# Kernel tuning notes

Hardware: AMD Instinct MI355X
Metric: run time of the kernel (lower is better)

Reference implementation:

```python
import jax, jax.numpy as jnp
import numpy as np

# Fixed feature-map grid sizes for a 640x480 input with strides (8,16,32)
LEVELS = [(8.0, 60, 80), (16.0, 30, 40), (32.0, 15, 20)]  # (stride, h, w) -> 6300 anchors
TOPK = 5


def make_anchors():
    pts, strs = [], []
    for stride, h, w in LEVELS:
        sx = np.arange(w, dtype=np.float32) + 0.5
        sy = np.arange(h, dtype=np.float32) + 0.5
        gy, gx = np.meshgrid(sy, sx, indexing='ij')
        pts.append(np.stack([gx, gy], -1).reshape(-1, 2))
        strs.append(np.full((h * w, 1), stride, dtype=np.float32))
    return jnp.asarray(np.concatenate(pts)), jnp.asarray(np.concatenate(strs))


def cxcywh_to_xyxy(b):
    cx, cy, w, h = b[..., 0], b[..., 1], b[..., 2], b[..., 3]
    return jnp.stack([cx - w / 2, cy - h / 2, cx + w / 2, cy + h / 2], axis=-1)


def giou_elementwise(a, b):
    # a, b: [..., 4] xyxy; elementwise GIoU (== diag of pairwise GIoU)
    lt = jnp.maximum(a[..., :2], b[..., :2])
    rb = jnp.minimum(a[..., 2:], b[..., 2:])
    wh = jnp.maximum(rb - lt, 0.0)
    inter = wh[..., 0] * wh[..., 1]
    area_a = (a[..., 2] - a[..., 0]) * (a[..., 3] - a[..., 1])
    area_b = (b[..., 2] - b[..., 0]) * (b[..., 3] - b[..., 1])
    union = area_a + area_b - inter
    iou = inter / union
    lt_c = jnp.minimum(a[..., :2], b[..., :2])
    rb_c = jnp.maximum(a[..., 2:], b[..., 2:])
    wh_c = jnp.maximum(rb_c - lt_c, 0.0)
    area_c = wh_c[..., 0] * wh_c[..., 1]
    return iou - (area_c - union) / area_c


def setup_inputs() -> dict:
    key = jax.random.key(0)
    k1, k2, k3, k4 = jax.random.split(key, 4)
    B = 256
    pred_boxes = jax.random.normal(k1, (B, 4, 6300), dtype=jnp.float32)
    pred_scores = jax.random.normal(k2, (B, 10, 6300), dtype=jnp.float32)
    u = jax.random.uniform(k3, (B, 4), dtype=jnp.float32)
    targets_bbox = jnp.stack([u[:, 0] * 640.0, u[:, 1] * 480.0,
                              u[:, 2] * 200.0 + 10.0, u[:, 3] * 200.0 + 10.0], axis=-1)
    targets_cls = jax.random.randint(k4, (B,), 0, 10)
    return {"pred_boxes": pred_boxes, "pred_scores": pred_scores,
            "targets_bbox": targets_bbox, "targets_cls": targets_cls}


def reference(pred_boxes, pred_scores, targets_bbox, targets_cls):
    pb = jnp.transpose(pred_boxes, (0, 2, 1))   # [B, A, 4]
    ps = jnp.transpose(pred_scores, (0, 2, 1))  # [B, A, C]
    B, A, C = ps.shape
    anchors, stride_t = make_anchors()  # [A,2], [A,1]

    # Box decode
    dxdy, twth = pb[..., :2], pb[..., 2:]
    pred_cxcy = (anchors[None] + dxdy) * stride_t[None]
    pred_wh = jnp.exp(jnp.minimum(twth, 10.0)) * stride_t[None]
    decoded = jnp.concatenate([pred_cxcy, pred_wh], axis=-1)  # [B,A,4]

    # Top-k closest anchors to GT center
    anchor_centers = anchors[None] * stride_t[None]             # [1,A,2]
    dist = jnp.linalg.norm(anchor_centers - targets_bbox[:, None, :2], axis=-1)  # [B,A]
    _, topk_idx = jax.lax.top_k(-dist, TOPK)                    # [B,K], smallest distances

    # GIoU box loss on matched anchors
    pos_pred = jnp.take_along_axis(decoded, topk_idx[..., None], axis=1)  # [B,K,4]
    pred_xyxy = cxcywh_to_xyxy(pos_pred)
    gt_xyxy = cxcywh_to_xyxy(targets_bbox)[:, None, :]          # [B,1,4]
    giou = giou_elementwise(pred_xyxy, jnp.broadcast_to(gt_xyxy, pred_xyxy.shape))
    loss_box = jnp.mean(1.0 - giou, axis=1).mean()

    # Scatter target scores
    bi = jnp.arange(B)[:, None]
    target_scores = jnp.zeros_like(ps).at[bi, topk_idx, targets_cls[:, None]].set(1.0)

    # Focal loss (BCE-with-logits base)
    bce = jnp.maximum(ps, 0.0) - ps * target_scores + jnp.log1p(jnp.exp(-jnp.abs(ps)))
    pt = jnp.exp(-bce)
    focal = 0.25 * (1.0 - pt) ** 2 * bce
    loss_cls = focal.sum() / B

    total = 5.0 * loss_box + 1.0 * loss_cls
    return total, loss_box, loss_cls
```

## Files before the change

kernel.cpp:

```cpp
#include <hip/hip_runtime.h>
#include <float.h>

#define B_SZ 256
#define N_ANCH 6300
#define N_CLS 10
#define TOPK_K 5


__device__ __forceinline__ void anchor_geom(int a, float& gx, float& gy, float& stride) {
    if (a < 4800) {
        stride = 8.0f;
        int x = a % 80, y = a / 80;
        gx = x + 0.5f; gy = y + 0.5f;
    } else if (a < 6000) {
        int r = a - 4800;
        stride = 16.0f;
        int x = r % 40, y = r / 40;
        gx = x + 0.5f; gy = y + 0.5f;
    } else {
        int r = a - 6000;
        stride = 32.0f;
        int x = r % 20, y = r / 20;
        gx = x + 0.5f; gy = y + 0.5f;
    }
}

__device__ __forceinline__ float focal0_fast(float s) {
    const float LOG2E = 1.4426950408889634f;
    const float LN2   = 0.6931471805599453f;
    float a   = fabsf(s);
    float u   = __builtin_amdgcn_exp2f(-a * LOG2E);
    float opu = 1.0f + u;
    float l   = __builtin_amdgcn_logf(opu) * LN2;
    float bce = fmaxf(s, 0.0f) + l;
    float r   = __builtin_amdgcn_rcpf(opu);
    float num = (s >= 0.0f) ? 1.0f : u;
    float sg  = num * r;
    return 0.25f * sg * sg * bce;
}


__global__ __launch_bounds__(256)
void topk_box_kernel(const float* __restrict__ pb,
                     const float* __restrict__ ps,
                     const float* __restrict__ tb,
                     const int*   __restrict__ tc,
                     double* __restrict__ wbox,
                     double* __restrict__ wcorr)
{
    const int b   = blockIdx.x;
    const int tid = threadIdx.x;

    const float txc = tb[b * 4 + 0];
    const float tyc = tb[b * 4 + 1];

    unsigned long long best[TOPK_K];
    #pragma unroll
    for (int k = 0; k < TOPK_K; ++k) best[k] = ~0ull;

    for (int a = tid; a < N_ANCH; a += 256) {
        float gx, gy, st;
        anchor_geom(a, gx, gy, st);
        float dx = __fsub_rn(__fmul_rn(gx, st), txc);
        float dy = __fsub_rn(__fmul_rn(gy, st), tyc);
        float d2 = __fadd_rn(__fmul_rn(dx, dx), __fmul_rn(dy, dy));
        float d  = sqrtf(d2);
        unsigned long long key =
            ((unsigned long long)__float_as_uint(d) << 32) | (unsigned int)a;
        if (key < best[TOPK_K - 1]) {
            best[TOPK_K - 1] = key;
            #pragma unroll
            for (int k = TOPK_K - 1; k > 0; --k) {
                unsigned long long lo = best[k - 1], hi = best[k];
                bool sw = hi < lo;
                best[k - 1] = sw ? hi : lo;
                best[k]     = sw ? lo : hi;
            }
        }
    }

    __shared__ unsigned long long wmin[4];
    __shared__ unsigned long long ssel[TOPK_K];
    int ptr = 0;
    for (int p = 0; p < TOPK_K; ++p) {
        unsigned long long cand = (ptr < TOPK_K) ? best[ptr] : ~0ull;
        unsigned long long m = cand;
        #pragma unroll
        for (int off = 32; off > 0; off >>= 1) {
            unsigned long long o = __shfl_xor(m, off, 64);
            m = (o < m) ? o : m;
        }
        if ((tid & 63) == 0) wmin[tid >> 6] = m;
        __syncthreads();
        if (tid == 0) {
            unsigned long long m01 = (wmin[0] < wmin[1]) ? wmin[0] : wmin[1];
            unsigned long long m23 = (wmin[2] < wmin[3]) ? wmin[2] : wmin[3];
            ssel[p] = (m01 < m23) ? m01 : m23;
        }
        __syncthreads();
        if (ptr < TOPK_K && cand == ssel[p]) ptr++;
    }

    __shared__ double sbox[TOPK_K], scorr[TOPK_K];
    if (tid < TOPK_K) {
        const int a = (int)(ssel[tid] & 0xffffffffu);
        float gx, gy, st;
        anchor_geom(a, gx, gy, st);

        const int base = b * 4 * N_ANCH + a;
        float ddx = pb[base + 0 * N_ANCH];
        float ddy = pb[base + 1 * N_ANCH];
        float tw  = pb[base + 2 * N_ANCH];
        float th  = pb[base + 3 * N_ANCH];

        float cx = (gx + ddx) * st;
        float cy = (gy + ddy) * st;
        float w  = expf(fminf(tw, 10.0f)) * st;
        float h  = expf(fminf(th, 10.0f)) * st;

        float ax0 = cx - w * 0.5f, ay0 = cy - h * 0.5f;
        float ax1 = cx + w * 0.5f, ay1 = cy + h * 0.5f;

        float gcx = tb[b * 4 + 0], gcy = tb[b * 4 + 1];
        float gw  = tb[b * 4 + 2], gh  = tb[b * 4 + 3];
        float bx0 = gcx - gw * 0.5f, by0 = gcy - gh * 0.5f;
        float bx1 = gcx + gw * 0.5f, by1 = gcy + gh * 0.5f;

        float ltx = fmaxf(ax0, bx0), lty = fmaxf(ay0, by0);
        float rbx = fminf(ax1, bx1), rby = fminf(ay1, by1);
        float iw = fmaxf(rbx - ltx, 0.0f), ih = fmaxf(rby - lty, 0.0f);
        float inter = iw * ih;
        float areaA = (ax1 - ax0) * (ay1 - ay0);
        float areaB = (bx1 - bx0) * (by1 - by0);
        float uni = areaA + areaB - inter;
        float iou = inter / uni;
        float ccx0 = fminf(ax0, bx0), ccy0 = fminf(ay0, by0);
        float ccx1 = fmaxf(ax1, bx1), ccy1 = fmaxf(ay1, by1);
        float cw = fmaxf(ccx1 - ccx0, 0.0f), ch = fmaxf(ccy1 - ccy0, 0.0f);
        float areaC = cw * ch;
        float giou = iou - (areaC - uni) / areaC;
        sbox[tid] = (double)(1.0f - giou);

        const int cls = tc[b];
        float s = ps[b * (N_CLS * N_ANCH) + cls * N_ANCH + a];
        scorr[tid] = (double)focal0_fast(-s) - (double)focal0_fast(s);
    }
    __syncthreads();
    if (tid == 0) {
        double bs = 0.0, cs = 0.0;
        for (int k = 0; k < TOPK_K; ++k) { bs += sbox[k]; cs += scorr[k]; }
        wbox[b]  = bs;
        wcorr[b] = cs;
    }
}


#define FOCAL_BLOCKS 2048

__global__ __launch_bounds__(256)
void focal_sum_kernel(const float4* __restrict__ ps4, int n4,
                      double* __restrict__ part)
{
    double acc = 0.0;
    const int stride = gridDim.x * blockDim.x;
    for (int i = blockIdx.x * blockDim.x + threadIdx.x; i < n4; i += stride) {
        float4 v = ps4[i];
        float fs = focal0_fast(v.x) + focal0_fast(v.y)
                 + focal0_fast(v.z) + focal0_fast(v.w);
        acc += (double)fs;
    }
    __shared__ double sacc[256];
    sacc[threadIdx.x] = acc;
    __syncthreads();
    for (int s = 128; s > 0; s >>= 1) {
        if (threadIdx.x < s) sacc[threadIdx.x] += sacc[threadIdx.x + s];
        __syncthreads();
    }
    if (threadIdx.x == 0) part[blockIdx.x] = sacc[0];
}


__global__ __launch_bounds__(256)
void finalize_kernel(const double* __restrict__ part,
                     const double* __restrict__ wbox,
                     const double* __restrict__ wcorr,
                     float* __restrict__ out)
{
    const int tid = threadIdx.x;
    double a = 0.0;
    for (int i = tid; i < FOCAL_BLOCKS; i += 256) a += part[i];
    double bsum = wbox[tid];
    double csum = wcorr[tid];

    __shared__ double s1[256], s2[256], s3[256];
    s1[tid] = a; s2[tid] = bsum; s3[tid] = csum;
    __syncthreads();
    for (int s = 128; s > 0; s >>= 1) {
        if (tid < s) {
            s1[tid] += s1[tid + s];
            s2[tid] += s2[tid + s];
            s3[tid] += s3[tid + s];
        }
        __syncthreads();
    }
    if (tid == 0) {
        double loss_cls = (s1[0] + s3[0]) / (double)B_SZ;
        double loss_box = s2[0] / (double)(B_SZ * TOPK_K);
        out[0] = (float)(5.0 * loss_box + loss_cls);
        out[1] = (float)loss_box;
        out[2] = (float)loss_cls;
    }
}


extern "C" void kernel_launch(void* const* d_in, const int* in_sizes, int n_in,
                              void* d_out, int out_size, void* d_ws, size_t ws_size,
                              hipStream_t stream) {
    const float* pb = (const float*)d_in[0];
    const float* ps = (const float*)d_in[1];
    const float* tb = (const float*)d_in[2];
    const int*   tc = (const int*)d_in[3];
    float* out = (float*)d_out;

    double* part  = (double*)d_ws;
    double* wbox  = part + FOCAL_BLOCKS;
    double* wcorr = wbox + B_SZ;

    topk_box_kernel<<<B_SZ, 256, 0, stream>>>(pb, ps, tb, tc, wbox, wcorr);

    const int n4 = (B_SZ * N_CLS * N_ANCH) / 4;
    focal_sum_kernel<<<FOCAL_BLOCKS, 256, 0, stream>>>((const float4*)ps, n4, part);

    finalize_kernel<<<1, 256, 0, stream>>>(part, wbox, wcorr, out);
}
```

Measured before the change: 122.5 us.

## Fuse top-k, focal sum and finalize into one kernel with atomic last-block reduction

Merges the three kernels into a single launch. The first 2048 blocks compute the focal sum and the last 256 blocks do the per-image top-k and GIoU work. Each block adds its partials into global doubles with atomics, and the last block to finish, detected by an atomic counter, writes the final losses. This removes two kernel launches and lets the small top-k work overlap with the bandwidth-bound focal pass. In exchange it adds a memset launch, contention on the double atomics, and a final sum whose order is nondeterministic.

New measurement: 214.9 us. +75.5%, slower.

```diff
diff --git a/kernel.cpp b/kernel.cpp
--- a/kernel.cpp
+++ b/kernel.cpp
@@ -5,6 +5,10 @@
 #define N_ANCH 6300
 #define N_CLS 10
 #define TOPK_K 5
+
+#define FOCAL_BLOCKS 2048
+#define TOTAL_BLOCKS (FOCAL_BLOCKS + B_SZ)
+
 
 
 __device__ __forceinline__ void anchor_geom(int a, float& gx, float& gy, float& stride) {
@@ -41,174 +45,157 @@
 
 
 __global__ __launch_bounds__(256)
-void topk_box_kernel(const float* __restrict__ pb,
-                     const float* __restrict__ ps,
-                     const float* __restrict__ tb,
-                     const int*   __restrict__ tc,
-                     double* __restrict__ wbox,
-                     double* __restrict__ wcorr)
+void fused_loss_kernel(const float*  __restrict__ pb,
+                       const float*  __restrict__ ps,
+                       const float*  __restrict__ tb,
+                       const int*    __restrict__ tc,
+                       double* __restrict__ acc,
+                       unsigned int* __restrict__ counter,
+                       float* __restrict__ out)
 {
-    const int b   = blockIdx.x;
+    const int blk = blockIdx.x;
     const int tid = threadIdx.x;
 
-    const float txc = tb[b * 4 + 0];
-    const float tyc = tb[b * 4 + 1];
-
-    unsigned long long best[TOPK_K];
-    #pragma unroll
-    for (int k = 0; k < TOPK_K; ++k) best[k] = ~0ull;
-
-    for (int a = tid; a < N_ANCH; a += 256) {
-        float gx, gy, st;
-        anchor_geom(a, gx, gy, st);
-        float dx = __fsub_rn(__fmul_rn(gx, st), txc);
-        float dy = __fsub_rn(__fmul_rn(gy, st), tyc);
-        float d2 = __fadd_rn(__fmul_rn(dx, dx), __fmul_rn(dy, dy));
-        float d  = sqrtf(d2);
-        unsigned long long key =
-            ((unsigned long long)__float_as_uint(d) << 32) | (unsigned int)a;
-        if (key < best[TOPK_K - 1]) {
-            best[TOPK_K - 1] = key;
-            #pragma unroll
-            for (int k = TOPK_K - 1; k > 0; --k) {
-                unsigned long long lo = best[k - 1], hi = best[k];
-                bool sw = hi < lo;
-                best[k - 1] = sw ? hi : lo;
-                best[k]     = sw ? lo : hi;
-            }
-        }
-    }
-
+    double p_focal = 0.0, p_box = 0.0, p_corr = 0.0;
+
+    __shared__ double sacc[256];
     __shared__ unsigned long long wmin[4];
     __shared__ unsigned long long ssel[TOPK_K];
-    int ptr = 0;
-    for (int p = 0; p < TOPK_K; ++p) {
-        unsigned long long cand = (ptr < TOPK_K) ? best[ptr] : ~0ull;
-        unsigned long long m = cand;
+    __shared__ double sbox[TOPK_K], scorr[TOPK_K];
+
+    if (blk < FOCAL_BLOCKS) {
+        const float4* ps4 = (const float4*)ps;
+        const int n4 = (B_SZ * N_CLS * N_ANCH) / 4;
+        const int stride = FOCAL_BLOCKS * 256;
+        double a = 0.0;
+        for (int i = blk * 256 + tid; i < n4; i += stride) {
+            float4 v = ps4[i];
+            float fs = focal0_fast(v.x) + focal0_fast(v.y)
+                     + focal0_fast(v.z) + focal0_fast(v.w);
+            a += (double)fs;
+        }
+        sacc[tid] = a;
+        __syncthreads();
+        for (int s = 128; s > 0; s >>= 1) {
+            if (tid < s) sacc[tid] += sacc[tid + s];
+            __syncthreads();
+        }
+        p_focal = sacc[0];
+    } else {
+        const int b = blk - FOCAL_BLOCKS;
+        const float txc = tb[b * 4 + 0];
+        const float tyc = tb[b * 4 + 1];
+
+        unsigned long long best[TOPK_K];
         #pragma unroll
-        for (int off = 32; off > 0; off >>= 1) {
-            unsigned long long o = __shfl_xor(m, off, 64);
-            m = (o < m) ? o : m;
-        }
-        if ((tid & 63) == 0) wmin[tid >> 6] = m;
+        for (int k = 0; k < TOPK_K; ++k) best[k] = ~0ull;
+
+        for (int a = tid; a < N_ANCH; a += 256) {
+            float gx, gy, st;
+            anchor_geom(a, gx, gy, st);
+            float dx = __fsub_rn(__fmul_rn(gx, st), txc);
+            float dy = __fsub_rn(__fmul_rn(gy, st), tyc);
+            float d2 = __fadd_rn(__fmul_rn(dx, dx), __fmul_rn(dy, dy));
+            float d  = sqrtf(d2);
+            unsigned long long key =
+                ((unsigned long long)__float_as_uint(d) << 32) | (unsigned int)a;
+            if (key < best[TOPK_K - 1]) {
+                best[TOPK_K - 1] = key;
+                #pragma unroll
+                for (int k = TOPK_K - 1; k > 0; --k) {
+                    unsigned long long lo = best[k - 1], hi = best[k];
+                    bool sw = hi < lo;
+                    best[k - 1] = sw ? hi : lo;
+                    best[k]     = sw ? lo : hi;
+                }
+            }
+        }
+
+        int ptr = 0;
+        for (int p = 0; p < TOPK_K; ++p) {
+            unsigned long long cand = (ptr < TOPK_K) ? best[ptr] : ~0ull;
+            unsigned long long m = cand;
+            #pragma unroll
+            for (int off = 32; off > 0; off >>= 1) {
+                unsigned long long o = __shfl_xor(m, off, 64);
+                m = (o < m) ? o : m;
+            }
+            if ((tid & 63) == 0) wmin[tid >> 6] = m;
+            __syncthreads();
+            if (tid == 0) {
+                unsigned long long m01 = (wmin[0] < wmin[1]) ? wmin[0] : wmin[1];
+                unsigned long long m23 = (wmin[2] < wmin[3]) ? wmin[2] : wmin[3];
+                ssel[p] = (m01 < m23) ? m01 : m23;
+            }
+            __syncthreads();
+            if (ptr < TOPK_K && cand == ssel[p]) ptr++;
+        }
+
+        if (tid < TOPK_K) {
+            const int a = (int)(ssel[tid] & 0xffffffffu);
+            float gx, gy, st;
+            anchor_geom(a, gx, gy, st);
+
+            const int base = b * 4 * N_ANCH + a;
+            float ddx = pb[base + 0 * N_ANCH];
+            float ddy = pb[base + 1 * N_ANCH];
+            float tw  = pb[base + 2 * N_ANCH];
+            float th  = pb[base + 3 * N_ANCH];
+
+            float cx = (gx + ddx) * st;
+            float cy = (gy + ddy) * st;
+            float w  = expf(fminf(tw, 10.0f)) * st;
+            float h  = expf(fminf(th, 10.0f)) * st;
+
+            float ax0 = cx - w * 0.5f, ay0 = cy - h * 0.5f;
+            float ax1 = cx + w * 0.5f, ay1 = cy + h * 0.5f;
+
+            float gcx = tb[b * 4 + 0], gcy = tb[b * 4 + 1];
+            float gw  = tb[b * 4 + 2], gh  = tb[b * 4 + 3];
+            float bx0 = gcx - gw * 0.5f, by0 = gcy - gh * 0.5f;
+            float bx1 = gcx + gw * 0.5f, by1 = gcy + gh * 0.5f;
+
+            float ltx = fmaxf(ax0, bx0), lty = fmaxf(ay0, by0);
+            float rbx = fminf(ax1, bx1), rby = fminf(ay1, by1);
+            float iw = fmaxf(rbx - ltx, 0.0f), ih = fmaxf(rby - lty, 0.0f);
+            float inter = iw * ih;
+            float areaA = (ax1 - ax0) * (ay1 - ay0);
+            float areaB = (bx1 - bx0) * (by1 - by0);
+            float uni = areaA + areaB - inter;
+            float iou = inter / uni;
+            float ccx0 = fminf(ax0, bx0), ccy0 = fminf(ay0, by0);
+            float ccx1 = fmaxf(ax1, bx1), ccy1 = fmaxf(ay1, by1);
+            float cw = fmaxf(ccx1 - ccx0, 0.0f), ch = fmaxf(ccy1 - ccy0, 0.0f);
+            float areaC = cw * ch;
+            float giou = iou - (areaC - uni) / areaC;
+            sbox[tid] = (double)(1.0f - giou);
+
+            const int cls = tc[b];
+            float s = ps[b * (N_CLS * N_ANCH) + cls * N_ANCH + a];
+            scorr[tid] = (double)focal0_fast(-s) - (double)focal0_fast(s);
+        }
         __syncthreads();
         if (tid == 0) {
-            unsigned long long m01 = (wmin[0] < wmin[1]) ? wmin[0] : wmin[1];
-            unsigned long long m23 = (wmin[2] < wmin[3]) ? wmin[2] : wmin[3];
-            ssel[p] = (m01 < m23) ? m01 : m23;
-        }
-        __syncthreads();
-        if (ptr < TOPK_K && cand == ssel[p]) ptr++;
+            for (int k = 0; k < TOPK_K; ++k) { p_box += sbox[k]; p_corr += scorr[k]; }
+        }
     }
 
-    __shared__ double sbox[TOPK_K], scorr[TOPK_K];
-    if (tid < TOPK_K) {
-        const int a = (int)(ssel[tid] & 0xffffffffu);
-        float gx, gy, st;
-        anchor_geom(a, gx, gy, st);
-
-        const int base = b * 4 * N_ANCH + a;
-        float ddx = pb[base + 0 * N_ANCH];
-        float ddy = pb[base + 1 * N_ANCH];
-        float tw  = pb[base + 2 * N_ANCH];
-        float th  = pb[base + 3 * N_ANCH];
-
-        float cx = (gx + ddx) * st;
-        float cy = (gy + ddy) * st;
-        float w  = expf(fminf(tw, 10.0f)) * st;
-        float h  = expf(fminf(th, 10.0f)) * st;
-
-        float ax0 = cx - w * 0.5f, ay0 = cy - h * 0.5f;
-        float ax1 = cx + w * 0.5f, ay1 = cy + h * 0.5f;
-
-        float gcx = tb[b * 4 + 0], gcy = tb[b * 4 + 1];
-        float gw  = tb[b * 4 + 2], gh  = tb[b * 4 + 3];
-        float bx0 = gcx - gw * 0.5f, by0 = gcy - gh * 0.5f;
-        float bx1 = gcx + gw * 0.5f, by1 = gcy + gh * 0.5f;
-
-        float ltx = fmaxf(ax0, bx0), lty = fmaxf(ay0, by0);
-        float rbx = fminf(ax1, bx1), rby = fminf(ay1, by1);
-        float iw = fmaxf(rbx - ltx, 0.0f), ih = fmaxf(rby - lty, 0.0f);
-        float inter = iw * ih;
-        float areaA = (ax1 - ax0) * (ay1 - ay0);
-        float areaB = (bx1 - bx0) * (by1 - by0);
-        float uni = areaA + areaB - inter;
-        float iou = inter / uni;
-        float ccx0 = fminf(ax0, bx0), ccy0 = fminf(ay0, by0);
-        float ccx1 = fmaxf(ax1, bx1), ccy1 = fmaxf(ay1, by1);
-        float cw = fmaxf(ccx1 - ccx0, 0.0f), ch = fmaxf(ccy1 - ccy0, 0.0f);
-        float areaC = cw * ch;
-        float giou = iou - (areaC - uni) / areaC;
-        sbox[tid] = (double)(1.0f - giou);
-
-        const int cls = tc[b];
-        float s = ps[b * (N_CLS * N_ANCH) + cls * N_ANCH + a];
-        scorr[tid] = (double)focal0_fast(-s) - (double)focal0_fast(s);
-    }
-    __syncthreads();
     if (tid == 0) {
-        double bs = 0.0, cs = 0.0;
-        for (int k = 0; k < TOPK_K; ++k) { bs += sbox[k]; cs += scorr[k]; }
-        wbox[b]  = bs;
-        wcorr[b] = cs;
-    }
-}
-
-
-#define FOCAL_BLOCKS 2048
-
-__global__ __launch_bounds__(256)
-void focal_sum_kernel(const float4* __restrict__ ps4, int n4,
-                      double* __restrict__ part)
-{
-    double acc = 0.0;
-    const int stride = gridDim.x * blockDim.x;
-    for (int i = blockIdx.x * blockDim.x + threadIdx.x; i < n4; i += stride) {
-        float4 v = ps4[i];
-        float fs = focal0_fast(v.x) + focal0_fast(v.y)
-                 + focal0_fast(v.z) + focal0_fast(v.w);
-        acc += (double)fs;
-    }
-    __shared__ double sacc[256];
-    sacc[threadIdx.x] = acc;
-    __syncthreads();
-    for (int s = 128; s > 0; s >>= 1) {
-        if (threadIdx.x < s) sacc[threadIdx.x] += sacc[threadIdx.x + s];
-        __syncthreads();
-    }
-    if (threadIdx.x == 0) part[blockIdx.x] = sacc[0];
-}
-
-
-__global__ __launch_bounds__(256)
-void finalize_kernel(const double* __restrict__ part,
-                     const double* __restrict__ wbox,
-                     const double* __restrict__ wcorr,
-                     float* __restrict__ out)
-{
-    const int tid = threadIdx.x;
-    double a = 0.0;
-    for (int i = tid; i < FOCAL_BLOCKS; i += 256) a += part[i];
-    double bsum = wbox[tid];
-    double csum = wcorr[tid];
-
-    __shared__ double s1[256], s2[256], s3[256];
-    s1[tid] = a; s2[tid] = bsum; s3[tid] = csum;
-    __syncthreads();
-    for (int s = 128; s > 0; s >>= 1) {
-        if (tid < s) {
-            s1[tid] += s1[tid + s];
-            s2[tid] += s2[tid + s];
-            s3[tid] += s3[tid + s];
-        }
-        __syncthreads();
-    }
-    if (tid == 0) {
-        double loss_cls = (s1[0] + s3[0]) / (double)B_SZ;
-        double loss_box = s2[0] / (double)(B_SZ * TOPK_K);
-        out[0] = (float)(5.0 * loss_box + loss_cls);
-        out[1] = (float)loss_box;
-        out[2] = (float)loss_cls;
+        atomicAdd(&acc[0], p_focal);
+        atomicAdd(&acc[1], p_box);
+        atomicAdd(&acc[2], p_corr);
+        __threadfence();
+        unsigned int old = atomicAdd(counter, 1u);
+        if (old == (unsigned int)(TOTAL_BLOCKS - 1)) {
+            double f = atomicAdd(&acc[0], 0.0);
+            double bx = atomicAdd(&acc[1], 0.0);
+            double cr = atomicAdd(&acc[2], 0.0);
+            double loss_cls = (f + cr) / (double)B_SZ;
+            double loss_box = bx / (double)(B_SZ * TOPK_K);
+            out[0] = (float)(5.0 * loss_box + loss_cls);
+            out[1] = (float)loss_box;
+            out[2] = (float)loss_cls;
+        }
     }
 }
 
@@ -222,14 +209,10 @@
     const int*   tc = (const int*)d_in[3];
     float* out = (float*)d_out;
 
-    double* part  = (double*)d_ws;
-    double* wbox  = part + FOCAL_BLOCKS;
-    double* wcorr = wbox + B_SZ;
-
-    topk_box_kernel<<<B_SZ, 256, 0, stream>>>(pb, ps, tb, tc, wbox, wcorr);
-
-    const int n4 = (B_SZ * N_CLS * N_ANCH) / 4;
-    focal_sum_kernel<<<FOCAL_BLOCKS, 256, 0, stream>>>((const float4*)ps, n4, part);
-
-    finalize_kernel<<<1, 256, 0, stream>>>(part, wbox, wcorr, out);
-}
+    double*       acc     = (double*)d_ws;
+    unsigned int* counter = (unsigned int*)((char*)d_ws + 24);
+
+    hipMemsetAsync(d_ws, 0, 64, stream);
+
+    fused_loss_kernel<<<TOTAL_BLOCKS, 256, 0, stream>>>(pb, ps, tb, tc, acc, counter, out);
+}
```
